# Kernel optimization log

Measured on AMD Instinct MI355X. Metric: run time of the kernel, lower is better.

The kernel has to match this reference:

```python
import jax, jax.numpy as jnp
import numpy as np

H = 128          # hidden_dim
L = 10           # num_iterations
NC = 8000        # check nodes
NV = 16000       # var nodes
E = 60000        # edges per direction
INPUT_SCALE = 0.1
LN_EPS = 1e-6


def _glorot(key, shape):
    fan_in, fan_out = shape[0], shape[-1]
    lim = np.sqrt(6.0 / (fan_in + fan_out))
    return jax.random.uniform(key, shape, jnp.float32, -lim, lim)


def _ln(x, g, b):
    m = jnp.mean(x, axis=-1, keepdims=True)
    v = jnp.var(x, axis=-1, keepdims=True)
    return g * (x - m) / jnp.sqrt(v + LN_EPS) + b


def _gru(x, h, W, U, b):
    # Keras GRUCell, reset_after=True; gate order: z (update), r (reset), h (candidate)
    xa = x @ W + b[0]            # [N, 3H]
    ha = h @ U + b[1]            # [N, 3H]
    z = jax.nn.sigmoid(xa[:, :H] + ha[:, :H])
    r = jax.nn.sigmoid(xa[:, H:2 * H] + ha[:, H:2 * H])
    hh = jnp.tanh(xa[:, 2 * H:] + r * ha[:, 2 * H:])
    return z * h + (1.0 - z) * hh


def setup_inputs() -> dict:
    key = jax.random.key(0)
    ks = jax.random.split(key, 24)
    d = {
        'check_feats': jax.random.normal(ks[0], (NC, 1), jnp.float32),
        'var_feats': jax.random.normal(ks[1], (NV, 1), jnp.float32),
        'c2v_src': jax.random.randint(ks[2], (E,), 0, NC, jnp.int32),
        'c2v_tgt': jax.random.randint(ks[3], (E,), 0, NV, jnp.int32),
        'v2c_src': jax.random.randint(ks[4], (E,), 0, NV, jnp.int32),
        'v2c_tgt': jax.random.randint(ks[5], (E,), 0, NC, jnp.int32),
        # input transforms (Dense 1->H) + LayerNorm params
        'Wc_in': _glorot(ks[6], (1, H)), 'bc_in': jnp.zeros((H,), jnp.float32),
        'Wv_in': _glorot(ks[7], (1, H)), 'bv_in': jnp.zeros((H,), jnp.float32),
        'gc_ln': jnp.ones((H,), jnp.float32), 'bc_ln': jnp.zeros((H,), jnp.float32),
        'gv_ln': jnp.ones((H,), jnp.float32), 'bv_ln': jnp.zeros((H,), jnp.float32),
        # SimpleConv message Dense(2H->H) per receiving node set
        'Wmsg_c': _glorot(ks[8], (2 * H, H)), 'bmsg_c': jnp.zeros((H,), jnp.float32),
        'Wmsg_v': _glorot(ks[9], (2 * H, H)), 'bmsg_v': jnp.zeros((H,), jnp.float32),
        # NextStateFromConcat Dense(2H->H)
        'Wns_c': _glorot(ks[10], (2 * H, H)), 'bns_c': jnp.zeros((H,), jnp.float32),
        'Wns_v': _glorot(ks[11], (2 * H, H)), 'bns_v': jnp.zeros((H,), jnp.float32),
        # GRU cells: kernel [H,3H], recurrent [H,3H], bias [2,3H]
        'Wg_c': _glorot(ks[12], (H, 3 * H)), 'Ug_c': _glorot(ks[13], (H, 3 * H)),
        'bg_c': jnp.zeros((2, 3 * H), jnp.float32),
        'Wg_v': _glorot(ks[14], (H, 3 * H)), 'Ug_v': _glorot(ks[15], (H, 3 * H)),
        'bg_v': jnp.zeros((2, 3 * H), jnp.float32),
        # final predictor Dense(H->1), bias = logit(p_error)
        'Wf': _glorot(ks[16], (H, 1)),
        'bf': jnp.full((1,), np.log((4.0 / NV) / (1 - 4.0 / NV)), jnp.float32),
    }
    return d


def reference(check_feats, var_feats, c2v_src, c2v_tgt, v2c_src, v2c_tgt,
              Wc_in, bc_in, Wv_in, bv_in, gc_ln, bc_ln, gv_ln, bv_ln,
              Wmsg_c, bmsg_c, Wmsg_v, bmsg_v, Wns_c, bns_c, Wns_v, bns_v,
              Wg_c, Ug_c, bg_c, Wg_v, Ug_v, bg_v, Wf, bf):
    hc = _ln((INPUT_SCALE * check_feats) @ Wc_in + bc_in, gc_ln, bc_ln)  # [NC,H]
    hv = _ln((INPUT_SCALE * var_feats) @ Wv_in + bv_in, gv_ln, bv_ln)    # [NV,H]
    for _ in range(L):
        # v_to_c SimpleConv: concat(sender var state, receiver check state) -> Dense+ELU -> scatter-sum
        m_vc = jax.nn.elu(jnp.concatenate([hv[v2c_src], hc[v2c_tgt]], axis=-1) @ Wmsg_c + bmsg_c)
        agg_c = jax.ops.segment_sum(m_vc, v2c_tgt, num_segments=NC)
        # c_to_v SimpleConv
        m_cv = jax.nn.elu(jnp.concatenate([hc[c2v_src], hv[c2v_tgt]], axis=-1) @ Wmsg_v + bmsg_v)
        agg_v = jnp.asarray(jax.ops.segment_sum(m_cv, c2v_tgt, num_segments=NV))
        # NextStateFromConcat: Dense(concat(old_state, pooled)) + ELU
        upd_c = jax.nn.elu(jnp.concatenate([hc, agg_c], axis=-1) @ Wns_c + bns_c)
        upd_v = jax.nn.elu(jnp.concatenate([hv, agg_v], axis=-1) @ Wns_v + bns_v)
        # GRU state update (update info is the input, prev state is the hidden state)
        hc = _gru(upd_c, hc, Wg_c, Ug_c, bg_c)
        hv = _gru(upd_v, hv, Wg_v, Ug_v, bg_v)
    # dropout is identity at inference; final Dense(H->1), squeeze
    return (hv @ Wf + bf)[:, 0]
```

## Files before the change

kernel.cpp:

```cpp
#include <hip/hip_runtime.h>
#include <hip/hip_bf16.h>
#include <math.h>

#define Hdim 128
#define NCn  8000
#define NVn  16000
#define NE   60000
#define LITERS 10
#define NCB16 500
#define NVB16 1000
#define NCB32 250
#define NVB32 500
#define PREPB 1408
#define SSRC_CAP 2048

typedef __attribute__((ext_vector_type(8))) short s8v;
typedef __attribute__((ext_vector_type(4))) float f4v;

__device__ __forceinline__ float fexp(float x) { return __expf(x); }
__device__ __forceinline__ float elu_f(float x) { return x > 0.0f ? x : (fexp(x) - 1.0f); }
__device__ __forceinline__ float sigm_f(float x) {
    return __builtin_amdgcn_rcpf(1.0f + fexp(-x));
}
__device__ __forceinline__ float tanh_f(float x) {
    return 1.0f - 2.0f * __builtin_amdgcn_rcpf(1.0f + fexp(2.0f * x));
}
__device__ __forceinline__ unsigned short f2b(float x) {
    __hip_bfloat16 h = __float2bfloat16(x); return *(unsigned short*)&h;
}
__device__ __forceinline__ float b2f(unsigned short u) {
    __hip_bfloat16 h; *(unsigned short*)&h = u; return __bfloat162float(h);
}

__global__ void prep_init(const float* __restrict__ Wmsg_c, const float* __restrict__ Wmsg_v,
                          const float* __restrict__ Wns_c,  const float* __restrict__ Wns_v,
                          const float* __restrict__ Wg_c, const float* __restrict__ Ug_c,
                          const float* __restrict__ Wg_v, const float* __restrict__ Ug_v,
                          unsigned short* __restrict__ Fmsg_c, unsigned short* __restrict__ Fmsg_v,
                          unsigned short* __restrict__ Fns_c,  unsigned short* __restrict__ Fns_v,
                          unsigned short* __restrict__ Fcat_c, unsigned short* __restrict__ Fuh_c,
                          unsigned short* __restrict__ Fcat_v, unsigned short* __restrict__ Fuh_v,
                          const float* __restrict__ cf, const float* __restrict__ vf,
                          const float* __restrict__ Wc, const float* __restrict__ bc,
                          const float* __restrict__ Wv, const float* __restrict__ bv,
                          const float* __restrict__ gc, const float* __restrict__ bcl,
                          const float* __restrict__ gv, const float* __restrict__ bvl,
                          float* __restrict__ hc, float* __restrict__ hv) {
    if (blockIdx.x < PREPB) {
        int idx = blockIdx.x * 256 + threadIdx.x;
        const int S1 = 4 * 32768;
        const int S2 = S1 + 2 * 98304;
        const int S3 = S2 + 2 * 16384;
        if (idx < S1) {
            int seg = idx >> 15, t = idx & 32767;
            const float* W = (seg == 0) ? Wmsg_c : (seg == 1) ? Wmsg_v : (seg == 2) ? Wns_c : Wns_v;
            unsigned short* outw = (seg == 0) ? Fmsg_c : (seg == 1) ? Fmsg_v : (seg == 2) ? Fns_c : Fns_v;
            int j = t & 7, lane = (t >> 3) & 63, t2 = t >> 9;
            int f = t2 & 7, kt = t2 >> 3;
            int n = f * 16 + (lane & 15), k = kt * 32 + (lane >> 4) * 8 + j;
            outw[t] = f2b(W[(size_t)k * 128 + n]);
        } else if (idx < S2) {
            int q = idx - S1;
            int seg = q / 98304, t = q - seg * 98304;
            const float* Wg = seg ? Wg_v : Wg_c;
            const float* Ug = seg ? Ug_v : Ug_c;
            unsigned short* outw = seg ? Fcat_v : Fcat_c;
            int j = t & 7, lane = (t >> 3) & 63, t2 = t >> 9;
            int f = t2 % 24, kt = t2 / 24;
            int n = f * 16 + (lane & 15), k = kt * 32 + (lane >> 4) * 8 + j;
            outw[t] = f2b((k < 128) ? Ug[(size_t)k * 384 + n] : Wg[(size_t)(k - 128) * 384 + n]);
        } else if (idx < S3) {
            int q = idx - S2;
            int seg = q >> 14, t = q & 16383;
            const float* Ug = seg ? Ug_v : Ug_c;
            unsigned short* outw = seg ? Fuh_v : Fuh_c;
            int j = t & 7, lane = (t >> 3) & 63, t2 = t >> 9;
            int f = t2 & 7, kt = t2 >> 3;
            int n = f * 16 + (lane & 15), k = kt * 32 + (lane >> 4) * 8 + j;
            outw[t] = f2b(Ug[(size_t)k * 384 + 256 + n]);
        }
        return;
    }
    int node = (blockIdx.x - PREPB) * 4 + (threadIdx.x >> 6);
    int lane = threadIdx.x & 63;
    const float *Win, *bin, *g, *bl;
    float f;
    float* outp;
    if (node < NCn) {
        f = cf[node]; Win = Wc; bin = bc; g = gc; bl = bcl;
        outp = hc + (size_t)node * Hdim;
    } else {
        int n2 = node - NCn;
        f = vf[n2]; Win = Wv; bin = bv; g = gv; bl = bvl;
        outp = hv + (size_t)n2 * Hdim;
    }
    f *= 0.1f;
    float x0 = f * Win[lane] + bin[lane];
    float x1 = f * Win[lane + 64] + bin[lane + 64];
    float s = x0 + x1;
    float sq = x0 * x0 + x1 * x1;
    #pragma unroll
    for (int off = 32; off > 0; off >>= 1) {
        s += __shfl_xor(s, off);
        sq += __shfl_xor(sq, off);
    }
    float m = s * (1.0f / 128.0f);
    float v = sq * (1.0f / 128.0f) - m * m;
    float inv = 1.0f / sqrtf(v + 1e-6f);
    outp[lane]      = g[lane]      * (x0 - m) * inv + bl[lane];
    outp[lane + 64] = g[lane + 64] * (x1 - m) * inv + bl[lane + 64];
}

__global__ void zero_int_kernel(int* __restrict__ p, int n) {
    int i = blockIdx.x * blockDim.x + threadIdx.x;
    if (i < n) p[i] = 0;
}
__global__ void hist_kernel(const int* __restrict__ tgt_c, const int* __restrict__ tgt_v,
                            int* __restrict__ cnt_c, int* __restrict__ cnt_v) {
    int e = blockIdx.x * blockDim.x + threadIdx.x;
    if (e >= NE) return;
    atomicAdd(&cnt_c[tgt_c[e]], 1);
    atomicAdd(&cnt_v[tgt_v[e]], 1);
}
__launch_bounds__(1024)
__global__ void scan2_kernel(const int* __restrict__ cnt_c, int* __restrict__ rp_c,
                             const int* __restrict__ cnt_v, int* __restrict__ rp_v) {
    const int* cnt = blockIdx.x ? cnt_v : cnt_c;
    int* rowptr = blockIdx.x ? rp_v : rp_c;
    const int n = blockIdx.x ? NVn : NCn;
    __shared__ int part[1024];
    int t = threadIdx.x;
    int chunk = (n + 1023) >> 10;
    int base = t * chunk;
    int s = 0;
    for (int i = 0; i < chunk; i++) { int idx = base + i; if (idx < n) s += cnt[idx]; }
    part[t] = s;
    __syncthreads();
    for (int off = 1; off < 1024; off <<= 1) {
        int u = (t >= off) ? part[t - off] : 0;
        __syncthreads();
        part[t] += u;
        __syncthreads();
    }
    int run = part[t] - s;
    for (int i = 0; i < chunk; i++) {
        int idx = base + i;
        if (idx < n) { rowptr[idx] = run; run += cnt[idx]; }
    }
    if (t == 0) rowptr[n] = part[1023];
}
__global__ void fill_kernel(const int* __restrict__ tgt_c, const int* __restrict__ tgt_v,
                            const int* __restrict__ src_c, const int* __restrict__ src_v,
                            const int* __restrict__ rp_c, const int* __restrict__ rp_v,
                            int* __restrict__ fill_c, int* __restrict__ fill_v,
                            int* __restrict__ srcs_c, int* __restrict__ srcs_v) {
    int e = blockIdx.x * blockDim.x + threadIdx.x;
    if (e >= NE) return;
    int tc = tgt_c[e];
    srcs_c[rp_c[tc] + atomicAdd(&fill_c[tc], 1)] = src_c[e];
    int tv = tgt_v[e];
    srcs_v[rp_v[tv] + atomicAdd(&fill_v[tv], 1)] = src_v[e];
}

__launch_bounds__(256)
__global__ void pq_init(const float* __restrict__ hc, const float* __restrict__ hv,
                        const unsigned short* __restrict__ Fmsg_c, const unsigned short* __restrict__ Fmsg_v,
                        const float* __restrict__ bmsg_c, const float* __restrict__ bmsg_v,
                        unsigned short* __restrict__ Pv_w, unsigned short* __restrict__ Qc_w,
                        unsigned short* __restrict__ Pc_w, unsigned short* __restrict__ Qv_w) {
    __shared__ unsigned short sA[32 * 136];
    const int bid = blockIdx.x;
    const int isV = (bid >= NCB32) ? 1 : 0;
    const int blockM = (isV ? (bid - NCB32) : bid) * 32;
    const float* h = isV ? hv : hc;
    const unsigned short* FP = isV ? Fmsg_c : Fmsg_v;
    const unsigned short* FQ = isV ? Fmsg_v : Fmsg_c;
    const float* bq = isV ? bmsg_v : bmsg_c;
    unsigned short* Pw = isV ? Pv_w : Pc_w;
    unsigned short* Qw = isV ? Qv_w : Qc_w;

    const int tid = threadIdx.x;
    const int lane = tid & 63, wave = tid >> 6;
    const int quad = lane >> 4, l16 = lane & 15;
    {
        int rr = tid >> 3, cc = tid & 7;
        const float* hrow = &h[(size_t)(blockM + rr) * Hdim + cc * 16];
        f4v x0 = *(const f4v*)hrow;
        f4v x1 = *(const f4v*)(hrow + 4);
        f4v x2 = *(const f4v*)(hrow + 8);
        f4v x3 = *(const f4v*)(hrow + 12);
        s8v w0, w1;
        #pragma unroll
        for (int i = 0; i < 4; i++) {
            w0[i] = (short)f2b(x0[i]); w0[i + 4] = (short)f2b(x1[i]);
            w1[i] = (short)f2b(x2[i]); w1[i + 4] = (short)f2b(x3[i]);
        }
        *(s8v*)&sA[rr * 136 + cc * 16]     = w0;
        *(s8v*)&sA[rr * 136 + cc * 16 + 8] = w1;
    }
    __syncthreads();

    f4v accP[2][2], accQ[2][2];
    #pragma unroll
    for (int mt = 0; mt < 2; mt++)
        #pragma unroll
        for (int u = 0; u < 2; u++) { accP[mt][u] = (f4v){0.f,0.f,0.f,0.f}; accQ[mt][u] = (f4v){0.f,0.f,0.f,0.f}; }

    #pragma unroll
    for (int kt = 0; kt < 4; kt++) {
        s8v a0 = *(const s8v*)&sA[l16 * 136 + kt * 32 + quad * 8];
        s8v a1 = *(const s8v*)&sA[(16 + l16) * 136 + kt * 32 + quad * 8];
        #pragma unroll
        for (int u = 0; u < 2; u++) {
            int ct = wave * 2 + u;
            s8v bp = *(const s8v*)&FP[((size_t)(kt * 8 + ct) * 64 + lane) * 8];
            s8v bqv = *(const s8v*)&FQ[((size_t)((kt + 4) * 8 + ct) * 64 + lane) * 8];
            accP[0][u] = __builtin_amdgcn_mfma_f32_16x16x32_bf16(a0, bp, accP[0][u], 0, 0, 0);
            accP[1][u] = __builtin_amdgcn_mfma_f32_16x16x32_bf16(a1, bp, accP[1][u], 0, 0, 0);
            accQ[0][u] = __builtin_amdgcn_mfma_f32_16x16x32_bf16(a0, bqv, accQ[0][u], 0, 0, 0);
            accQ[1][u] = __builtin_amdgcn_mfma_f32_16x16x32_bf16(a1, bqv, accQ[1][u], 0, 0, 0);
        }
    }
    #pragma unroll
    for (int u = 0; u < 2; u++) {
        int col = (wave * 2 + u) * 16 + l16;
        float qbias = bq[col];
        #pragma unroll
        for (int mt = 0; mt < 2; mt++)
            #pragma unroll
            for (int reg = 0; reg < 4; reg++) {
                int row = blockM + mt * 16 + quad * 4 + reg;
                Pw[(size_t)row * Hdim + col] = f2b(accP[mt][u][reg]);
                Qw[(size_t)row * Hdim + col] = f2b(accQ[mt][u][reg] + qbias);
            }
    }
}

__launch_bounds__(256)
__global__ void node_fused(float* __restrict__ hc, float* __restrict__ hv,
                           const int* __restrict__ rp_c, const int* __restrict__ rp_v,
                           const int* __restrict__ srcs_c, const int* __restrict__ srcs_v,
                           const unsigned short* __restrict__ Pv_r, const unsigned short* __restrict__ Qc_r,
                           const unsigned short* __restrict__ Pc_r, const unsigned short* __restrict__ Qv_r,
                           unsigned short* __restrict__ Pv_w, unsigned short* __restrict__ Qc_w,
                           unsigned short* __restrict__ Pc_w, unsigned short* __restrict__ Qv_w,
                           const unsigned short* __restrict__ Fns_c, const float* __restrict__ bns_c,
                           const unsigned short* __restrict__ Fns_v, const float* __restrict__ bns_v,
                           const unsigned short* __restrict__ Fcat_c, const unsigned short* __restrict__ Fuh_c,
                           const unsigned short* __restrict__ Fcat_v, const unsigned short* __restrict__ Fuh_v,
                           const float* __restrict__ bg_c, const float* __restrict__ bg_v,
                           const unsigned short* __restrict__ Fmsg_c, const unsigned short* __restrict__ Fmsg_v,
                           const float* __restrict__ bmsg_c, const float* __restrict__ bmsg_v,
                           const float* __restrict__ Wf, const float* __restrict__ bf,
                           float* __restrict__ out, int do_pq, int vOnly) {
    __shared__ unsigned short sA[16 * 264];
    __shared__ int sSrc[SSRC_CAP];
    __shared__ int sRp[17];
    __shared__ float sRed[64];
    const int bid = blockIdx.x;
    const int isV = vOnly ? 1 : ((bid >= NCB16) ? 1 : 0);
    const int blockM = (vOnly ? bid : (isV ? (bid - NCB16) : bid)) * 16;
    float* h = isV ? hv : hc;
    const int* rp = isV ? rp_v : rp_c;
    const int* srcs = isV ? srcs_v : srcs_c;
    const unsigned short* Pr = isV ? Pc_r : Pv_r;
    const unsigned short* Qr = isV ? Qv_r : Qc_r;
    const unsigned short* Fns = isV ? Fns_v : Fns_c;
    const float* bns = isV ? bns_v : bns_c;
    const unsigned short* Fcat = isV ? Fcat_v : Fcat_c;
    const unsigned short* Fuh = isV ? Fuh_v : Fuh_c;
    const float* bg = isV ? bg_v : bg_c;
    const unsigned short* FP = isV ? Fmsg_c : Fmsg_v;
    const unsigned short* FQ = isV ? Fmsg_v : Fmsg_c;
    const float* bq = isV ? bmsg_v : bmsg_c;
    unsigned short* Pw = isV ? Pv_w : Pc_w;
    unsigned short* Qw = isV ? Qv_w : Qc_w;

    const int tid = threadIdx.x;
    const int lane = tid & 63, wave = tid >> 6;
    const int quad = lane >> 4, l16 = lane & 15;
    const int r = tid >> 4, ch = tid & 15;
    const int node = blockM + r;

    if (tid <= 16) sRp[tid] = rp[blockM + tid];
    const int eb = rp[blockM];
    {
        const int nE0 = rp[blockM + 16] - eb;
        const int nE = (nE0 < SSRC_CAP) ? nE0 : SSRC_CAP;
        for (int i = tid; i < nE; i += 256) sSrc[i] = srcs[eb + i];
    }
    {
        const float* hrow = &h[(size_t)node * Hdim + ch * 8];
        f4v h0 = *(const f4v*)hrow;
        f4v h1 = *(const f4v*)(hrow + 4);
        s8v hw;
        #pragma unroll
        for (int i = 0; i < 4; i++) { hw[i] = (short)f2b(h0[i]); hw[i + 4] = (short)f2b(h1[i]); }
        *(s8v*)&sA[r * 264 + ch * 8] = hw;
    }
    __syncthreads();

    {
        s8v q8 = *(const s8v*)&Qr[(size_t)node * Hdim + ch * 8];
        float qf[8], acc[8];
        #pragma unroll
        for (int i = 0; i < 8; i++) { qf[i] = b2f((unsigned short)q8[i]); acc[i] = 0.0f; }

        int j = sRp[r] - eb;
        const int e0 = sRp[r + 1] - eb;
        auto lsrc = [&](int jj) -> int {
            return (jj < SSRC_CAP) ? sSrc[jj] : srcs[eb + jj];
        };
        for (; j + 4 <= e0; j += 4) {
            int s0 = lsrc(j), s1 = lsrc(j + 1), s2 = lsrc(j + 2), s3 = lsrc(j + 3);
            s8v p0 = *(const s8v*)&Pr[(size_t)s0 * Hdim + ch * 8];
            s8v p1 = *(const s8v*)&Pr[(size_t)s1 * Hdim + ch * 8];
            s8v p2 = *(const s8v*)&Pr[(size_t)s2 * Hdim + ch * 8];
            s8v p3 = *(const s8v*)&Pr[(size_t)s3 * Hdim + ch * 8];
            #pragma unroll
            for (int i = 0; i < 8; i++) acc[i] += elu_f(b2f((unsigned short)p0[i]) + qf[i]);
            #pragma unroll
            for (int i = 0; i < 8; i++) acc[i] += elu_f(b2f((unsigned short)p1[i]) + qf[i]);
            #pragma unroll
            for (int i = 0; i < 8; i++) acc[i] += elu_f(b2f((unsigned short)p2[i]) + qf[i]);
            #pragma unroll
            for (int i = 0; i < 8; i++) acc[i] += elu_f(b2f((unsigned short)p3[i]) + qf[i]);
        }
        if (j + 2 <= e0) {
            int s0 = lsrc(j), s1 = lsrc(j + 1);
            s8v p0 = *(const s8v*)&Pr[(size_t)s0 * Hdim + ch * 8];
            s8v p1 = *(const s8v*)&Pr[(size_t)s1 * Hdim + ch * 8];
            #pragma unroll
            for (int i = 0; i < 8; i++) acc[i] += elu_f(b2f((unsigned short)p0[i]) + qf[i]);
            #pragma unroll
            for (int i = 0; i < 8; i++) acc[i] += elu_f(b2f((unsigned short)p1[i]) + qf[i]);
            j += 2;
        }
        if (j < e0) {
            int s0 = lsrc(j);
            s8v p0 = *(const s8v*)&Pr[(size_t)s0 * Hdim + ch * 8];
            #pragma unroll
            for (int i = 0; i < 8; i++) acc[i] += elu_f(b2f((unsigned short)p0[i]) + qf[i]);
        }
        s8v w;
        #pragma unroll
        for (int i = 0; i < 8; i++) w[i] = (short)f2b(acc[i]);
        *(s8v*)&sA[r * 264 + 128 + ch * 8] = w;
    }
    __syncthreads();

    f4v accA[2];
    accA[0] = (f4v){0.f,0.f,0.f,0.f};
    accA[1] = (f4v){0.f,0.f,0.f,0.f};
    #pragma unroll
    for (int kt = 0; kt < 8; kt++) {
        s8v a = *(const s8v*)&sA[l16 * 264 + kt * 32 + quad * 8];
        #pragma unroll
        for (int u = 0; u < 2; u++) {
            s8v b = *(const s8v*)&Fns[((size_t)(kt * 8 + wave * 2 + u) * 64 + lane) * 8];
            accA[u] = __builtin_amdgcn_mfma_f32_16x16x32_bf16(a, b, accA[u], 0, 0, 0);
        }
    }
    float updv[2][4];
    #pragma unroll
    for (int u = 0; u < 2; u++) {
        int col = (wave * 2 + u) * 16 + l16;
        float bb = bns[col];
        #pragma unroll
        for (int reg = 0; reg < 4; reg++)
            updv[u][reg] = elu_f(accA[u][reg] + bb);
    }
    __syncthreads();
    #pragma unroll
    for (int u = 0; u < 2; u++) {
        int col = (wave * 2 + u) * 16 + l16;
        #pragma unroll
        for (int reg = 0; reg < 4; reg++)
            sA[(quad * 4 + reg) * 264 + 128 + col] = f2b(updv[u][reg]);
    }
    __syncthreads();

    float hnv[2][4];
    #pragma unroll
    for (int u = 0; u < 2; u++) {
        const int j = wave * 2 + u;
        f4v sZ = (f4v){0.f,0.f,0.f,0.f};
        f4v sR = (f4v){0.f,0.f,0.f,0.f};
        f4v sH = (f4v){0.f,0.f,0.f,0.f};
        f4v hH = (f4v){0.f,0.f,0.f,0.f};
        #pragma unroll
        for (int kt = 0; kt < 8; kt++) {
            s8v a = *(const s8v*)&sA[l16 * 264 + kt * 32 + quad * 8];
            s8v bz = *(const s8v*)&Fcat[((size_t)(kt * 24 + j) * 64 + lane) * 8];
            s8v br = *(const s8v*)&Fcat[((size_t)(kt * 24 + 8 + j) * 64 + lane) * 8];
            s8v bh = *(const s8v*)&Fcat[((size_t)(kt * 24 + 16 + j) * 64 + lane) * 8];
            sZ = __builtin_amdgcn_mfma_f32_16x16x32_bf16(a, bz, sZ, 0, 0, 0);
            sR = __builtin_amdgcn_mfma_f32_16x16x32_bf16(a, br, sR, 0, 0, 0);
            sH = __builtin_amdgcn_mfma_f32_16x16x32_bf16(a, bh, sH, 0, 0, 0);
            if (kt < 4) {
                s8v bu = *(const s8v*)&Fuh[((size_t)(kt * 8 + j) * 64 + lane) * 8];
                hH = __builtin_amdgcn_mfma_f32_16x16x32_bf16(a, bu, hH, 0, 0, 0);
            }
        }
        const int t = j * 16 + l16;
        float bz2 = bg[t]       + bg[384 + t];
        float br2 = bg[128 + t] + bg[512 + t];
        float b0h = bg[256 + t];
        float b1h = bg[640 + t];
        #pragma unroll
        for (int reg = 0; reg < 4; reg++) {
            int row = blockM + quad * 4 + reg;
            float z = sigm_f(sZ[reg] + bz2);
            float rr = sigm_f(sR[reg] + br2);
            float hh = tanh_f((sH[reg] - hH[reg] + b0h) + rr * (hH[reg] + b1h));
            float hold = h[(size_t)row * Hdim + t];
            float hn = z * hold + (1.0f - z) * hh;
            if (do_pq) h[(size_t)row * Hdim + t] = hn;
            hnv[u][reg] = hn;
        }
    }

    if (!do_pq) {
        float wf0 = Wf[(wave * 2 + 0) * 16 + l16];
        float wf1 = Wf[(wave * 2 + 1) * 16 + l16];
        float part[4];
        #pragma unroll
        for (int reg = 0; reg < 4; reg++)
            part[reg] = hnv[0][reg] * wf0 + hnv[1][reg] * wf1;
        #pragma unroll
        for (int off = 1; off < 16; off <<= 1) {
            #pragma unroll
            for (int reg = 0; reg < 4; reg++)
                part[reg] += __shfl_xor(part[reg], off);
        }
        if (l16 == 0) {
            #pragma unroll
            for (int reg = 0; reg < 4; reg++)
                sRed[wave * 16 + quad * 4 + reg] = part[reg];
        }
        __syncthreads();
        if (tid < 16)
            out[blockM + tid] = sRed[tid] + sRed[16 + tid] + sRed[32 + tid] + sRed[48 + tid] + bf[0];
        return;
    }

    __syncthreads();
    #pragma unroll
    for (int u = 0; u < 2; u++) {
        int col = (wave * 2 + u) * 16 + l16;
        #pragma unroll
        for (int reg = 0; reg < 4; reg++)
            sA[(quad * 4 + reg) * 264 + col] = f2b(hnv[u][reg]);
    }
    __syncthreads();

    f4v accP[2], accQ[2];
    accP[0] = (f4v){0.f,0.f,0.f,0.f}; accP[1] = (f4v){0.f,0.f,0.f,0.f};
    accQ[0] = (f4v){0.f,0.f,0.f,0.f}; accQ[1] = (f4v){0.f,0.f,0.f,0.f};
    #pragma unroll
    for (int kt = 0; kt < 4; kt++) {
        s8v a = *(const s8v*)&sA[l16 * 264 + kt * 32 + quad * 8];
        #pragma unroll
        for (int u = 0; u < 2; u++) {
            int ct = wave * 2 + u;
            s8v bp = *(const s8v*)&FP[((size_t)(kt * 8 + ct) * 64 + lane) * 8];
            s8v bqv = *(const s8v*)&FQ[((size_t)((kt + 4) * 8 + ct) * 64 + lane) * 8];
            accP[u] = __builtin_amdgcn_mfma_f32_16x16x32_bf16(a, bp, accP[u], 0, 0, 0);
            accQ[u] = __builtin_amdgcn_mfma_f32_16x16x32_bf16(a, bqv, accQ[u], 0, 0, 0);
        }
    }
    #pragma unroll
    for (int u = 0; u < 2; u++) {
        int col = (wave * 2 + u) * 16 + l16;
        float qbias = bq[col];
        #pragma unroll
        for (int reg = 0; reg < 4; reg++) {
            int row = blockM + quad * 4 + reg;
            Pw[(size_t)row * Hdim + col] = f2b(accP[u][reg]);
            Qw[(size_t)row * Hdim + col] = f2b(accQ[u][reg] + qbias);
        }
    }
}

extern "C" void kernel_launch(void* const* d_in, const int* in_sizes, int n_in,
                              void* d_out, int out_size, void* d_ws, size_t ws_size,
                              hipStream_t stream) {
    const float* cf      = (const float*)d_in[0];
    const float* vf      = (const float*)d_in[1];
    const int*   c2v_src = (const int*)d_in[2];
    const int*   c2v_tgt = (const int*)d_in[3];
    const int*   v2c_src = (const int*)d_in[4];
    const int*   v2c_tgt = (const int*)d_in[5];
    const float* Wc_in   = (const float*)d_in[6];
    const float* bc_in   = (const float*)d_in[7];
    const float* Wv_in   = (const float*)d_in[8];
    const float* bv_in   = (const float*)d_in[9];
    const float* gc_ln   = (const float*)d_in[10];
    const float* bc_ln   = (const float*)d_in[11];
    const float* gv_ln   = (const float*)d_in[12];
    const float* bv_ln   = (const float*)d_in[13];
    const float* Wmsg_c  = (const float*)d_in[14];
    const float* bmsg_c  = (const float*)d_in[15];
    const float* Wmsg_v  = (const float*)d_in[16];
    const float* bmsg_v  = (const float*)d_in[17];
    const float* Wns_c   = (const float*)d_in[18];
    const float* bns_c   = (const float*)d_in[19];
    const float* Wns_v   = (const float*)d_in[20];
    const float* bns_v   = (const float*)d_in[21];
    const float* Wg_c    = (const float*)d_in[22];
    const float* Ug_c    = (const float*)d_in[23];
    const float* bg_c    = (const float*)d_in[24];
    const float* Wg_v    = (const float*)d_in[25];
    const float* Ug_v    = (const float*)d_in[26];
    const float* bg_v    = (const float*)d_in[27];
    const float* Wf      = (const float*)d_in[28];
    const float* bf      = (const float*)d_in[29];
    float* out = (float*)d_out;

    char* p = (char*)d_ws;
    #define CARVE(name, type, count) type* name = (type*)p; p += (((size_t)(count) * sizeof(type)) + 255) & ~(size_t)255;
    CARVE(hc,     float, NCn * Hdim)
    CARVE(hv,     float, NVn * Hdim)
    CARVE(Pv0,    unsigned short, NVn * Hdim)
    CARVE(Qc0,    unsigned short, NCn * Hdim)
    CARVE(Pc0,    unsigned short, NCn * Hdim)
    CARVE(Qv0,    unsigned short, NVn * Hdim)
    CARVE(Pv1,    unsigned short, NVn * Hdim)
    CARVE(Qc1,    unsigned short, NCn * Hdim)
    CARVE(Pc1,    unsigned short, NCn * Hdim)
    CARVE(Qv1,    unsigned short, NVn * Hdim)
    CARVE(Fmsg_c, unsigned short, 32768)
    CARVE(Fmsg_v, unsigned short, 32768)
    CARVE(Fns_c,  unsigned short, 32768)
    CARVE(Fns_v,  unsigned short, 32768)
    CARVE(Fcat_c, unsigned short, 98304)
    CARVE(Fuh_c,  unsigned short, 16384)
    CARVE(Fcat_v, unsigned short, 98304)
    CARVE(Fuh_v,  unsigned short, 16384)
    CARVE(rp_c,  int, NCn + 8)
    CARVE(rp_v,  int, NVn + 8)
    CARVE(srcs_c, int, NE)
    CARVE(srcs_v, int, NE)
    CARVE(cnts,  int, 48000)
    #undef CARVE
    int* cnt_c  = cnts;
    int* cnt_v  = cnts + NCn;
    int* fill_c = cnts + NCn + NVn;
    int* fill_v = cnts + 2 * NCn + NVn;

    prep_init<<<PREPB + 6000, 256, 0, stream>>>(
        Wmsg_c, Wmsg_v, Wns_c, Wns_v, Wg_c, Ug_c, Wg_v, Ug_v,
        Fmsg_c, Fmsg_v, Fns_c, Fns_v, Fcat_c, Fuh_c, Fcat_v, Fuh_v,
        cf, vf, Wc_in, bc_in, Wv_in, bv_in, gc_ln, bc_ln, gv_ln, bv_ln, hc, hv);
    zero_int_kernel<<<(48000 + 255) / 256, 256, 0, stream>>>(cnts, 48000);
    hist_kernel<<<(NE + 255) / 256, 256, 0, stream>>>(v2c_tgt, c2v_tgt, cnt_c, cnt_v);
    scan2_kernel<<<2, 1024, 0, stream>>>(cnt_c, rp_c, cnt_v, rp_v);
    fill_kernel<<<(NE + 255) / 256, 256, 0, stream>>>(v2c_tgt, c2v_tgt, v2c_src, c2v_src,
                                                      rp_c, rp_v, fill_c, fill_v, srcs_c, srcs_v);
    pq_init<<<NCB32 + NVB32, 256, 0, stream>>>(hc, hv, Fmsg_c, Fmsg_v, bmsg_c, bmsg_v,
                                               Pv0, Qc0, Pc0, Qv0);

    unsigned short* Pv_[2] = {Pv0, Pv1};
    unsigned short* Qc_[2] = {Qc0, Qc1};
    unsigned short* Pc_[2] = {Pc0, Pc1};
    unsigned short* Qv_[2] = {Qv0, Qv1};

    for (int it = 0; it < LITERS; it++) {
        int rd = it & 1, wr = rd ^ 1;
        int last = (it == LITERS - 1);
        node_fused<<<last ? NVB16 : (NCB16 + NVB16), 256, 0, stream>>>(
            hc, hv, rp_c, rp_v, srcs_c, srcs_v,
            Pv_[rd], Qc_[rd], Pc_[rd], Qv_[rd],
            Pv_[wr], Qc_[wr], Pc_[wr], Qv_[wr],
            Fns_c, bns_c, Fns_v, bns_v,
            Fcat_c, Fuh_c, Fcat_v, Fuh_v, bg_c, bg_v,
            Fmsg_c, Fmsg_v, bmsg_c, bmsg_v,
            Wf, bf, out, last ? 0 : 1, last ? 1 : 0);
    }
}
```

Measured before the change: 518.2 us.

## Merge setup kernels and drop shared-memory source staging in node kernel

Folds the counter zeroing into prep_init and fuses the CSR fill with the initial P/Q projection kernel, which removes two launches. In node_fused, the shared-memory staging of edge source indices and its barrier are dropped. Each thread now reads srcs directly, with gathers unrolled by 8 for more memory-level parallelism. The old hidden state is cached in shared memory for the GRU blend instead of being reloaded from global. The risk is that the fill blocks and P/Q blocks now run concurrently in one launch, and that direct srcs reads add global traffic.

```diff
diff --git a/kernel.cpp b/kernel.cpp
--- a/kernel.cpp
+++ b/kernel.cpp
@@ -12,7 +12,9 @@
 #define NCB32 250
 #define NVB32 500
 #define PREPB 1408
-#define SSRC_CAP 2048
+#define INITB 6000
+#define ZEROB 188
+#define FILLB 235
 
 typedef __attribute__((ext_vector_type(8))) short s8v;
 typedef __attribute__((ext_vector_type(4))) float f4v;
@@ -45,7 +47,13 @@
                           const float* __restrict__ Wv, const float* __restrict__ bv,
                           const float* __restrict__ gc, const float* __restrict__ bcl,
                           const float* __restrict__ gv, const float* __restrict__ bvl,
-                          float* __restrict__ hc, float* __restrict__ hv) {
+                          float* __restrict__ hc, float* __restrict__ hv,
+                          int* __restrict__ cnts) {
+    if (blockIdx.x >= PREPB + INITB) {
+        int i = (blockIdx.x - PREPB - INITB) * 256 + threadIdx.x;
+        if (i < 48000) cnts[i] = 0;
+        return;
+    }
     if (blockIdx.x < PREPB) {
         int idx = blockIdx.x * 256 + threadIdx.x;
         const int S1 = 4 * 32768;
@@ -111,10 +119,6 @@
     outp[lane + 64] = g[lane + 64] * (x1 - m) * inv + bl[lane + 64];
 }
 
-__global__ void zero_int_kernel(int* __restrict__ p, int n) {
-    int i = blockIdx.x * blockDim.x + threadIdx.x;
-    if (i < n) p[i] = 0;
-}
 __global__ void hist_kernel(const int* __restrict__ tgt_c, const int* __restrict__ tgt_v,
                             int* __restrict__ cnt_c, int* __restrict__ cnt_v) {
     int e = blockIdx.x * blockDim.x + threadIdx.x;
@@ -149,27 +153,29 @@
     }
     if (t == 0) rowptr[n] = part[1023];
 }
-__global__ void fill_kernel(const int* __restrict__ tgt_c, const int* __restrict__ tgt_v,
-                            const int* __restrict__ src_c, const int* __restrict__ src_v,
-                            const int* __restrict__ rp_c, const int* __restrict__ rp_v,
-                            int* __restrict__ fill_c, int* __restrict__ fill_v,
-                            int* __restrict__ srcs_c, int* __restrict__ srcs_v) {
-    int e = blockIdx.x * blockDim.x + threadIdx.x;
-    if (e >= NE) return;
-    int tc = tgt_c[e];
-    srcs_c[rp_c[tc] + atomicAdd(&fill_c[tc], 1)] = src_c[e];
-    int tv = tgt_v[e];
-    srcs_v[rp_v[tv] + atomicAdd(&fill_v[tv], 1)] = src_v[e];
-}
 
 __launch_bounds__(256)
-__global__ void pq_init(const float* __restrict__ hc, const float* __restrict__ hv,
+__global__ void fill_pq(const int* __restrict__ tgt_c, const int* __restrict__ tgt_v,
+                        const int* __restrict__ src_c, const int* __restrict__ src_v,
+                        const int* __restrict__ rp_c, const int* __restrict__ rp_v,
+                        int* __restrict__ fill_c, int* __restrict__ fill_v,
+                        int* __restrict__ srcs_c, int* __restrict__ srcs_v,
+                        const float* __restrict__ hc, const float* __restrict__ hv,
                         const unsigned short* __restrict__ Fmsg_c, const unsigned short* __restrict__ Fmsg_v,
                         const float* __restrict__ bmsg_c, const float* __restrict__ bmsg_v,
                         unsigned short* __restrict__ Pv_w, unsigned short* __restrict__ Qc_w,
                         unsigned short* __restrict__ Pc_w, unsigned short* __restrict__ Qv_w) {
+    if (blockIdx.x < FILLB) {
+        int e = blockIdx.x * 256 + threadIdx.x;
+        if (e >= NE) return;
+        int tc = tgt_c[e];
+        srcs_c[rp_c[tc] + atomicAdd(&fill_c[tc], 1)] = src_c[e];
+        int tv = tgt_v[e];
+        srcs_v[rp_v[tv] + atomicAdd(&fill_v[tv], 1)] = src_v[e];
+        return;
+    }
     __shared__ unsigned short sA[32 * 136];
-    const int bid = blockIdx.x;
+    const int bid = blockIdx.x - FILLB;
     const int isV = (bid >= NCB32) ? 1 : 0;
     const int blockM = (isV ? (bid - NCB32) : bid) * 32;
     const float* h = isV ? hv : hc;
@@ -254,8 +260,7 @@
                            const float* __restrict__ Wf, const float* __restrict__ bf,
                            float* __restrict__ out, int do_pq, int vOnly) {
     __shared__ unsigned short sA[16 * 264];
-    __shared__ int sSrc[SSRC_CAP];
-    __shared__ int sRp[17];
+    __shared__ float sHf[16 * 128];
     __shared__ float sRed[64];
     const int bid = blockIdx.x;
     const int isV = vOnly ? 1 : ((bid >= NCB16) ? 1 : 0);
@@ -282,54 +287,49 @@
     const int r = tid >> 4, ch = tid & 15;
     const int node = blockM + r;
 
-    if (tid <= 16) sRp[tid] = rp[blockM + tid];
-    const int eb = rp[blockM];
     {
-        const int nE0 = rp[blockM + 16] - eb;
-        const int nE = (nE0 < SSRC_CAP) ? nE0 : SSRC_CAP;
-        for (int i = tid; i < nE; i += 256) sSrc[i] = srcs[eb + i];
-    }
-    {
+        s8v q8 = *(const s8v*)&Qr[(size_t)node * Hdim + ch * 8];
         const float* hrow = &h[(size_t)node * Hdim + ch * 8];
         f4v h0 = *(const f4v*)hrow;
         f4v h1 = *(const f4v*)(hrow + 4);
+        int j = rp[node];
+        const int e0 = rp[node + 1];
+
         s8v hw;
         #pragma unroll
         for (int i = 0; i < 4; i++) { hw[i] = (short)f2b(h0[i]); hw[i + 4] = (short)f2b(h1[i]); }
         *(s8v*)&sA[r * 264 + ch * 8] = hw;
-    }
-    __syncthreads();
-
-    {
-        s8v q8 = *(const s8v*)&Qr[(size_t)node * Hdim + ch * 8];
+        *(f4v*)&sHf[r * 128 + ch * 8]     = h0;
+        *(f4v*)&sHf[r * 128 + ch * 8 + 4] = h1;
+
         float qf[8], acc[8];
         #pragma unroll
         for (int i = 0; i < 8; i++) { qf[i] = b2f((unsigned short)q8[i]); acc[i] = 0.0f; }
 
-        int j = sRp[r] - eb;
-        const int e0 = sRp[r + 1] - eb;
-        auto lsrc = [&](int jj) -> int {
-            return (jj < SSRC_CAP) ? sSrc[jj] : srcs[eb + jj];
-        };
-        for (; j + 4 <= e0; j += 4) {
-            int s0 = lsrc(j), s1 = lsrc(j + 1), s2 = lsrc(j + 2), s3 = lsrc(j + 3);
-            s8v p0 = *(const s8v*)&Pr[(size_t)s0 * Hdim + ch * 8];
-            s8v p1 = *(const s8v*)&Pr[(size_t)s1 * Hdim + ch * 8];
-            s8v p2 = *(const s8v*)&Pr[(size_t)s2 * Hdim + ch * 8];
-            s8v p3 = *(const s8v*)&Pr[(size_t)s3 * Hdim + ch * 8];
-            #pragma unroll
-            for (int i = 0; i < 8; i++) acc[i] += elu_f(b2f((unsigned short)p0[i]) + qf[i]);
-            #pragma unroll
-            for (int i = 0; i < 8; i++) acc[i] += elu_f(b2f((unsigned short)p1[i]) + qf[i]);
-            #pragma unroll
-            for (int i = 0; i < 8; i++) acc[i] += elu_f(b2f((unsigned short)p2[i]) + qf[i]);
-            #pragma unroll
-            for (int i = 0; i < 8; i++) acc[i] += elu_f(b2f((unsigned short)p3[i]) + qf[i]);
+        for (; j + 8 <= e0; j += 8) {
+            s8v p[8];
+            #pragma unroll
+            for (int b = 0; b < 8; b++)
+                p[b] = *(const s8v*)&Pr[(size_t)srcs[j + b] * Hdim + ch * 8];
+            #pragma unroll
+            for (int b = 0; b < 8; b++)
+                #pragma unroll
+                for (int i = 0; i < 8; i++) acc[i] += elu_f(b2f((unsigned short)p[b][i]) + qf[i]);
+        }
+        if (j + 4 <= e0) {
+            s8v p[4];
+            #pragma unroll
+            for (int b = 0; b < 4; b++)
+                p[b] = *(const s8v*)&Pr[(size_t)srcs[j + b] * Hdim + ch * 8];
+            #pragma unroll
+            for (int b = 0; b < 4; b++)
+                #pragma unroll
+                for (int i = 0; i < 8; i++) acc[i] += elu_f(b2f((unsigned short)p[b][i]) + qf[i]);
+            j += 4;
         }
         if (j + 2 <= e0) {
-            int s0 = lsrc(j), s1 = lsrc(j + 1);
-            s8v p0 = *(const s8v*)&Pr[(size_t)s0 * Hdim + ch * 8];
-            s8v p1 = *(const s8v*)&Pr[(size_t)s1 * Hdim + ch * 8];
+            s8v p0 = *(const s8v*)&Pr[(size_t)srcs[j] * Hdim + ch * 8];
+            s8v p1 = *(const s8v*)&Pr[(size_t)srcs[j + 1] * Hdim + ch * 8];
             #pragma unroll
             for (int i = 0; i < 8; i++) acc[i] += elu_f(b2f((unsigned short)p0[i]) + qf[i]);
             #pragma unroll
@@ -337,8 +337,7 @@
             j += 2;
         }
         if (j < e0) {
-            int s0 = lsrc(j);
-            s8v p0 = *(const s8v*)&Pr[(size_t)s0 * Hdim + ch * 8];
+            s8v p0 = *(const s8v*)&Pr[(size_t)srcs[j] * Hdim + ch * 8];
             #pragma unroll
             for (int i = 0; i < 8; i++) acc[i] += elu_f(b2f((unsigned short)p0[i]) + qf[i]);
         }
@@ -409,13 +408,13 @@
         float b1h = bg[640 + t];
         #pragma unroll
         for (int reg = 0; reg < 4; reg++) {
-            int row = blockM + quad * 4 + reg;
+            int rloc = quad * 4 + reg;
             float z = sigm_f(sZ[reg] + bz2);
             float rr = sigm_f(sR[reg] + br2);
             float hh = tanh_f((sH[reg] - hH[reg] + b0h) + rr * (hH[reg] + b1h));
-            float hold = h[(size_t)row * Hdim + t];
+            float hold = sHf[rloc * 128 + t];
             float hn = z * hold + (1.0f - z) * hh;
-            if (do_pq) h[(size_t)row * Hdim + t] = hn;
+            if (do_pq) h[(size_t)(blockM + rloc) * Hdim + t] = hn;
             hnv[u][reg] = hn;
         }
     }
@@ -548,17 +547,15 @@
     int* fill_c = cnts + NCn + NVn;
     int* fill_v = cnts + 2 * NCn + NVn;
 
-    prep_init<<<PREPB + 6000, 256, 0, stream>>>(
+    prep_init<<<PREPB + INITB + ZEROB, 256, 0, stream>>>(
         Wmsg_c, Wmsg_v, Wns_c, Wns_v, Wg_c, Ug_c, Wg_v, Ug_v,
         Fmsg_c, Fmsg_v, Fns_c, Fns_v, Fcat_c, Fuh_c, Fcat_v, Fuh_v,
-        cf, vf, Wc_in, bc_in, Wv_in, bv_in, gc_ln, bc_ln, gv_ln, bv_ln, hc, hv);
-    zero_int_kernel<<<(48000 + 255) / 256, 256, 0, stream>>>(cnts, 48000);
+        cf, vf, Wc_in, bc_in, Wv_in, bv_in, gc_ln, bc_ln, gv_ln, bv_ln, hc, hv, cnts);
     hist_kernel<<<(NE + 255) / 256, 256, 0, stream>>>(v2c_tgt, c2v_tgt, cnt_c, cnt_v);
     scan2_kernel<<<2, 1024, 0, stream>>>(cnt_c, rp_c, cnt_v, rp_v);
-    fill_kernel<<<(NE + 255) / 256, 256, 0, stream>>>(v2c_tgt, c2v_tgt, v2c_src, c2v_src,
-                                                      rp_c, rp_v, fill_c, fill_v, srcs_c, srcs_v);
-    pq_init<<<NCB32 + NVB32, 256, 0, stream>>>(hc, hv, Fmsg_c, Fmsg_v, bmsg_c, bmsg_v,
-                                               Pv0, Qc0, Pc0, Qv0);
+    fill_pq<<<FILLB + NCB32 + NVB32, 256, 0, stream>>>(
+        v2c_tgt, c2v_tgt, v2c_src, c2v_src, rp_c, rp_v, fill_c, fill_v, srcs_c, srcs_v,
+        hc, hv, Fmsg_c, Fmsg_v, bmsg_c, bmsg_v, Pv0, Qc0, Pc0, Qv0);
 
     unsigned short* Pv_[2] = {Pv0, Pv1};
     unsigned short* Qc_[2] = {Qc0, Qc1};
```

New measurement: 497.7 us. 4.0% less time.
